# Kernel optimization log

Hardware: AMD Instinct MI355X
Metric: run time of the kernel (lower is better)

The kernel has to match this reference:

```python
import jax, jax.numpy as jnp
import numpy as np

B, D, H, W, C = 2, 128, 128, 128, 4
OD, OH, OW = 96, 96, 96
RANK = 3


def setup_inputs() -> dict:
    key = jax.random.key(0)
    k1, k2 = jax.random.split(key)
    inputs = jax.random.normal(k1, (B, D, H, W, C), dtype=jnp.float32)
    # continuous sample coords in [0, size-1] per spatial dim
    scale = jnp.array([D - 1, H - 1, W - 1], dtype=jnp.float32)
    sample_coords = jax.random.uniform(k2, (B, OD, OH, OW, RANK), dtype=jnp.float32) * scale
    return {"inputs": inputs, "sample_coords": sample_coords}


def _pyramid_combination(samples, w_0, w_1):
    # recursive weighted blend over 2^rank corner samples (matches TF module)
    if len(w_0) == 1:
        return samples[0] * w_1[0] + samples[1] * w_0[0]
    f_0 = _pyramid_combination(samples[::2], w_0[:-1], w_1[:-1])
    f_1 = _pyramid_combination(samples[1::2], w_0[:-1], w_1[:-1])
    return f_0 * w_1[-1] + f_1 * w_0[-1]


def reference(inputs, sample_coords):
    # inputs: [B, D, H, W, C]; sample_coords: [B, od, oh, ow, 3]
    in_spatial = inputs.shape[1:-1]
    rank = len(in_spatial)
    batch = inputs.shape[0]

    coords = [sample_coords[..., d] for d in range(rank)]          # each [B, od, oh, ow]
    base = [jnp.floor(c) for c in coords]
    # ZERO boundary -> replicate clamp of integer coords
    floor_i = [jnp.clip(b.astype(jnp.int32), 0, in_spatial[d] - 1) for d, b in enumerate(base)]
    ceil_i = [jnp.clip((b + 1.0).astype(jnp.int32), 0, in_spatial[d] - 1) for d, b in enumerate(base)]

    # ZERO-boundary weights use the CLAMPED corner coords (faithful to source)
    w_0 = [(c - f.astype(jnp.float32))[..., None] for c, f in zip(coords, floor_i)]
    w_1 = [(ce.astype(jnp.float32) - c)[..., None] for c, ce in zip(coords, ceil_i)]

    bids = jnp.arange(batch)[:, None, None, None]                  # broadcast batch ids
    sc = (floor_i, ceil_i)

    samples = []
    for i in range(2 ** rank):
        bits = [(i >> (rank - 1 - d)) & 1 for d in range(rank)]    # dim-0 is most significant bit
        idx = [sc[bits[d]][d] for d in range(rank)]
        samples.append(inputs[bids, idx[0], idx[1], idx[2]])       # [B, od, oh, ow, C]

    return _pyramid_combination(samples, w_0, w_1)
```

## Files before the change

### kernel.cpp

```cpp
#include <hip/hip_runtime.h>
#include <hip/hip_fp16.h>


constexpr int D = 128, H = 128, W = 128;
constexpr int OD = 96, OH = 96, OW = 96;
constexpr int VOX_PER_B = OD * OH * OW;
constexpr int NVOX = 2 * VOX_PER_B;

constexpr int NBINS = 1024;
constexpr int NB1 = 216;
constexpr int SPB = 8192;
constexpr int GT = 512;
constexpr int TILE_ELEMS = 9 * 5 * 128;

constexpr size_t OFF_MATRIX  = 0;
constexpr size_t OFF_NCNT    = (size_t)NB1 * NBINS * 4;
constexpr size_t OFF_BASE    = OFF_NCNT + NBINS * 4;
constexpr size_t OFF_RECORDS = OFF_BASE + NBINS * 4;
constexpr size_t WS_REQUIRED = OFF_RECORDS + (size_t)NVOX * 16;

__device__ __forceinline__ int bin_of(float cz, float cy, int b) {
    int z0 = min(max((int)floorf(cz), 0), D - 1);
    int y0 = min(max((int)floorf(cy), 0), H - 1);
    return (((b << 4) | (z0 >> 3)) << 5) | (y0 >> 2);
}

__device__ __forceinline__ float4 f4_fma(float w, float4 a, float4 acc) {
    acc.x = fmaf(w, a.x, acc.x);
    acc.y = fmaf(w, a.y, acc.y);
    acc.z = fmaf(w, a.z, acc.z);
    acc.w = fmaf(w, a.w, acc.w);
    return acc;
}
__device__ __forceinline__ float4 f4_scale(float w, float4 a) {
    return make_float4(w * a.x, w * a.y, w * a.z, w * a.w);
}

__device__ __forceinline__ float4 xblend(uint2 p0, uint2 p1, float w0, float w1) {
    const __half2 a0 = *(const __half2*)&p0.x;
    const __half2 a1 = *(const __half2*)&p0.y;
    const __half2 b0 = *(const __half2*)&p1.x;
    const __half2 b1 = *(const __half2*)&p1.y;
    const float2 A0 = __half22float2(a0), A1 = __half22float2(a1);
    const float2 B0 = __half22float2(b0), B1 = __half22float2(b1);
    float4 o;
    o.x = fmaf(w1, B0.x, w0 * A0.x);
    o.y = fmaf(w1, B0.y, w0 * A0.y);
    o.z = fmaf(w1, B1.x, w0 * A1.x);
    o.w = fmaf(w1, B1.y, w0 * A1.y);
    return o;
}

__global__ __launch_bounds__(1024) void hist_kernel(const float* __restrict__ coords,
                                                    unsigned* __restrict__ matrix) {
    __shared__ unsigned cnt[NBINS];
    const int t = threadIdx.x;
    cnt[t] = 0;
    __syncthreads();
    const int s0 = blockIdx.x * SPB;
#pragma unroll
    for (int j = 0; j < 8; j++) {
        const int s = s0 + j * 1024 + t;
        const float cz = coords[s * 3 + 0];
        const float cy = coords[s * 3 + 1];
        const int b = (s >= VOX_PER_B) ? 1 : 0;
        atomicAdd(&cnt[bin_of(cz, cy, b)], 1u);
    }
    __syncthreads();
    matrix[blockIdx.x * NBINS + t] = cnt[t];
}

__global__ __launch_bounds__(256) void scanA_kernel(unsigned* __restrict__ matrix,
                                                    unsigned* __restrict__ ncnt) {
    const int k = blockIdx.x;
    const int t = threadIdx.x;
    const unsigned v = (t < NB1) ? matrix[t * NBINS + k] : 0u;
    __shared__ unsigned s[256];
    s[t] = v;
    __syncthreads();
    for (int off = 1; off < 256; off <<= 1) {
        unsigned u = (t >= off) ? s[t - off] : 0u;
        __syncthreads();
        s[t] += u;
        __syncthreads();
    }
    if (t < NB1) matrix[t * NBINS + k] = s[t] - v;
    if (t == 255) ncnt[k] = s[255];
}

__global__ __launch_bounds__(1024) void scanB_kernel(const unsigned* __restrict__ ncnt,
                                                     unsigned* __restrict__ base) {
    const int t = threadIdx.x;
    const unsigned v = ncnt[t];
    __shared__ unsigned s[NBINS];
    s[t] = v;
    __syncthreads();
    for (int off = 1; off < NBINS; off <<= 1) {
        unsigned u = (t >= off) ? s[t - off] : 0u;
        __syncthreads();
        s[t] += u;
        __syncthreads();
    }
    base[t] = s[t] - v;
}

__global__ __launch_bounds__(1024) void scatter_kernel(const float* __restrict__ coords,
                                                       const unsigned* __restrict__ matrix,
                                                       const unsigned* __restrict__ base,
                                                       float4* __restrict__ records) {
    __shared__ float4 rec[SPB];
    __shared__ unsigned short binid[SPB];
    __shared__ unsigned cnt[NBINS];
    __shared__ unsigned pref[NBINS];
    __shared__ unsigned gb[NBINS];
    const int t = threadIdx.x;
    const int blk = blockIdx.x;
    cnt[t] = 0;
    gb[t] = base[t] + matrix[blk * NBINS + t];
    __syncthreads();

    const int s0 = blk * SPB;
    float czr[8], cyr[8], cxr[8];
    unsigned rankr[8];
#pragma unroll
    for (int j = 0; j < 8; j++) {
        const int s = s0 + j * 1024 + t;
        czr[j] = coords[s * 3 + 0];
        cyr[j] = coords[s * 3 + 1];
        cxr[j] = coords[s * 3 + 2];
        const int b = (s >= VOX_PER_B) ? 1 : 0;
        rankr[j] = atomicAdd(&cnt[bin_of(czr[j], cyr[j], b)], 1u);
    }
    __syncthreads();

    pref[t] = cnt[t];
    __syncthreads();
    for (int off = 1; off < NBINS; off <<= 1) {
        unsigned u = (t >= off) ? pref[t - off] : 0u;
        __syncthreads();
        pref[t] += u;
        __syncthreads();
    }
    {
        unsigned ex = pref[t] - cnt[t];
        __syncthreads();
        pref[t] = ex;
    }
    __syncthreads();

#pragma unroll
    for (int j = 0; j < 8; j++) {
        const int s = s0 + j * 1024 + t;
        const int b = (s >= VOX_PER_B) ? 1 : 0;
        const int k = bin_of(czr[j], cyr[j], b);
        const unsigned slot = pref[k] + rankr[j];
        rec[slot] = make_float4(czr[j], cyr[j], cxr[j], __uint_as_float((unsigned)s));
        binid[slot] = (unsigned short)k;
    }
    __syncthreads();

#pragma unroll
    for (int j = 0; j < 8; j++) {
        const int i = j * 1024 + t;
        const int k = binid[i];
        records[gb[k] + (unsigned)(i - (int)pref[k])] = rec[i];
    }
}

__global__ __launch_bounds__(GT) void gather_kernel(
    const float* __restrict__ inp,
    const float4* __restrict__ records,
    const unsigned* __restrict__ base,
    const unsigned* __restrict__ ncnt,
    float4* __restrict__ out)
{
    __shared__ uint2 tile[TILE_ELEMS];
    const int k = ((blockIdx.x & 7) << 7) | (blockIdx.x >> 3);
    const int b  = k >> 9;
    const int zb = (k >> 5) & 15;
    const int yb = k & 31;
    const int t = threadIdx.x;

    const float4* bp = (const float4*)inp + ((size_t)b << 21);
    const int zlim = min(9, D - zb * 8);
    const int ylim = min(5, H - yb * 4);
    for (int i = t; i < TILE_ELEMS; i += GT) {
        const int z = i / 640;
        const int r = i - z * 640;
        const int y = r >> 7;
        const int x = r & 127;
        if (z < zlim && y < ylim) {
            const float4 v = bp[((zb * 8 + z) << 14) | ((yb * 4 + y) << 7) | x];
            const __half2 lo = __floats2half2_rn(v.x, v.y);
            const __half2 hi = __floats2half2_rn(v.z, v.w);
            tile[i] = make_uint2(*(const unsigned*)&lo, *(const unsigned*)&hi);
        }
    }
    __syncthreads();

    const unsigned st = base[k];
    const unsigned n = ncnt[k];
    const int zoff = zb * 8, yoff = yb * 4;
    for (unsigned i = st + t; i < st + n; i += GT) {
        const float4 r = records[i];
        const float cz = r.x, cy = r.y, cx = r.z;
        const unsigned idx = __float_as_uint(r.w);

        const int z0 = (int)floorf(cz);
        const int y0 = (int)floorf(cy);
        const int x0 = (int)floorf(cx);

        const float wz0 = (float)(z0 + 1) - cz, wz1 = cz - (float)z0;
        const float wy0 = (float)(y0 + 1) - cy, wy1 = cy - (float)y0;
        const float wx0 = (float)(x0 + 1) - cx, wx1 = cx - (float)x0;

        const int a00 = (z0 - zoff) * 640 + (y0 - yoff) * 128 + x0;
        const int a01 = a00 + 128;
        const int a10 = a00 + 640;
        const int a11 = a00 + 768;

        const float4 c00 = xblend(tile[a00], tile[a00 + 1], wx0, wx1);
        const float4 c01 = xblend(tile[a01], tile[a01 + 1], wx0, wx1);
        const float4 c10 = xblend(tile[a10], tile[a10 + 1], wx0, wx1);
        const float4 c11 = xblend(tile[a11], tile[a11 + 1], wx0, wx1);

        const float4 c0 = f4_fma(wy1, c01, f4_scale(wy0, c00));
        const float4 c1 = f4_fma(wy1, c11, f4_scale(wy0, c10));
        out[idx] = f4_fma(wz1, c1, f4_scale(wz0, c0));
    }
}

__global__ __launch_bounds__(256) void direct_kernel(const float* __restrict__ inp,
                                                     const float* __restrict__ coords,
                                                     float4* __restrict__ out) {
    const int idx = blockIdx.x * 256 + threadIdx.x;
    if (idx >= NVOX) return;
    const float cz = coords[idx * 3 + 0];
    const float cy = coords[idx * 3 + 1];
    const float cx = coords[idx * 3 + 2];
    const int b = (idx >= VOX_PER_B) ? 1 : 0;

    const int fz = (int)floorf(cz);
    const int fy = (int)floorf(cy);
    const int fx = (int)floorf(cx);
    const int z1 = min(max(fz + 1, 0), D - 1);
    const int y1 = min(max(fy + 1, 0), H - 1);
    const int x1 = min(max(fx + 1, 0), W - 1);
    const int z0 = min(max(fz, 0), D - 1);
    const int y0 = min(max(fy, 0), H - 1);
    const int x0 = min(max(fx, 0), W - 1);
    const float wz0 = (float)z1 - cz, wz1 = cz - (float)z0;
    const float wy0 = (float)y1 - cy, wy1 = cy - (float)y0;
    const float wx0 = (float)x1 - cx, wx1 = cx - (float)x0;
    const float4* bp = (const float4*)inp + ((size_t)b << 21);
    const int z0o = z0 << 14, z1o = z1 << 14;
    const int y0o = y0 << 7,  y1o = y1 << 7;
    const float4 s000 = bp[z0o | y0o | x0];
    const float4 s001 = bp[z0o | y0o | x1];
    const float4 s010 = bp[z0o | y1o | x0];
    const float4 s011 = bp[z0o | y1o | x1];
    const float4 s100 = bp[z1o | y0o | x0];
    const float4 s101 = bp[z1o | y0o | x1];
    const float4 s110 = bp[z1o | y1o | x0];
    const float4 s111 = bp[z1o | y1o | x1];
    float4 c00 = f4_fma(wx1, s001, f4_scale(wx0, s000));
    float4 c01 = f4_fma(wx1, s011, f4_scale(wx0, s010));
    float4 c10 = f4_fma(wx1, s101, f4_scale(wx0, s100));
    float4 c11 = f4_fma(wx1, s111, f4_scale(wx0, s110));
    float4 c0 = f4_fma(wy1, c01, f4_scale(wy0, c00));
    float4 c1 = f4_fma(wy1, c11, f4_scale(wy0, c10));
    out[idx] = f4_fma(wz1, c1, f4_scale(wz0, c0));
}

extern "C" void kernel_launch(void* const* d_in, const int* in_sizes, int n_in,
                              void* d_out, int out_size, void* d_ws, size_t ws_size,
                              hipStream_t stream) {
    const float* inp    = (const float*)d_in[0];
    const float* coords = (const float*)d_in[1];
    float4* out = (float4*)d_out;

    if (ws_size < WS_REQUIRED) {
        direct_kernel<<<(NVOX + 255) / 256, 256, 0, stream>>>(inp, coords, out);
        return;
    }

    char* ws = (char*)d_ws;
    unsigned* matrix  = (unsigned*)(ws + OFF_MATRIX);
    unsigned* ncnt    = (unsigned*)(ws + OFF_NCNT);
    unsigned* base    = (unsigned*)(ws + OFF_BASE);
    float4*   records = (float4*)(ws + OFF_RECORDS);

    hist_kernel   <<<NB1, 1024, 0, stream>>>(coords, matrix);
    scanA_kernel  <<<NBINS, 256, 0, stream>>>(matrix, ncnt);
    scanB_kernel  <<<1, 1024, 0, stream>>>(ncnt, base);
    scatter_kernel<<<NB1, 1024, 0, stream>>>(coords, matrix, base, records);
    gather_kernel <<<NBINS, GT, 0, stream>>>(inp, records, base, ncnt, out);
}
```

Before: 173.8 us.

## Replace histogram and scan passes with atomic-reserved fixed-capacity bins and packed records

Removes the separate histogram and two scan kernels. Each scatter block now reserves space in fixed-capacity per-bin slots using global atomics, and writes compact 12-byte records holding the sample index, local floor offsets and 16-bit quantized fractions. If a bin overflows, the sample is interpolated directly inside the scatter kernel. This cuts two kernel launches and one full pass over the coordinates, and shrinks record traffic. In exchange it quantizes the interpolation weights to 16 bits and adds a memset plus possible slow paths when a bin overflows.

```diff
diff --git a/kernel.cpp b/kernel.cpp
--- a/kernel.cpp
+++ b/kernel.cpp
@@ -8,22 +8,17 @@
 constexpr int NVOX = 2 * VOX_PER_B;
 
 constexpr int NBINS = 1024;
+constexpr int CAP = 2048;
 constexpr int NB1 = 216;
 constexpr int SPB = 8192;
 constexpr int GT = 512;
 constexpr int TILE_ELEMS = 9 * 5 * 128;
 
-constexpr size_t OFF_MATRIX  = 0;
-constexpr size_t OFF_NCNT    = (size_t)NB1 * NBINS * 4;
-constexpr size_t OFF_BASE    = OFF_NCNT + NBINS * 4;
-constexpr size_t OFF_RECORDS = OFF_BASE + NBINS * 4;
-constexpr size_t WS_REQUIRED = OFF_RECORDS + (size_t)NVOX * 16;
-
-__device__ __forceinline__ int bin_of(float cz, float cy, int b) {
-    int z0 = min(max((int)floorf(cz), 0), D - 1);
-    int y0 = min(max((int)floorf(cy), 0), H - 1);
-    return (((b << 4) | (z0 >> 3)) << 5) | (y0 >> 2);
-}
+struct Rec { unsigned w0, w1, w2; };
+
+constexpr size_t OFF_GCNT    = 0;
+constexpr size_t OFF_RECORDS = 4096;
+constexpr size_t WS_REQUIRED = OFF_RECORDS + (size_t)NBINS * CAP * 12;
 
 __device__ __forceinline__ float4 f4_fma(float w, float4 a, float4 acc) {
     acc.x = fmaf(w, a.x, acc.x);
@@ -51,195 +46,8 @@
     return o;
 }
 
-__global__ __launch_bounds__(1024) void hist_kernel(const float* __restrict__ coords,
-                                                    unsigned* __restrict__ matrix) {
-    __shared__ unsigned cnt[NBINS];
-    const int t = threadIdx.x;
-    cnt[t] = 0;
-    __syncthreads();
-    const int s0 = blockIdx.x * SPB;
-#pragma unroll
-    for (int j = 0; j < 8; j++) {
-        const int s = s0 + j * 1024 + t;
-        const float cz = coords[s * 3 + 0];
-        const float cy = coords[s * 3 + 1];
-        const int b = (s >= VOX_PER_B) ? 1 : 0;
-        atomicAdd(&cnt[bin_of(cz, cy, b)], 1u);
-    }
-    __syncthreads();
-    matrix[blockIdx.x * NBINS + t] = cnt[t];
-}
-
-__global__ __launch_bounds__(256) void scanA_kernel(unsigned* __restrict__ matrix,
-                                                    unsigned* __restrict__ ncnt) {
-    const int k = blockIdx.x;
-    const int t = threadIdx.x;
-    const unsigned v = (t < NB1) ? matrix[t * NBINS + k] : 0u;
-    __shared__ unsigned s[256];
-    s[t] = v;
-    __syncthreads();
-    for (int off = 1; off < 256; off <<= 1) {
-        unsigned u = (t >= off) ? s[t - off] : 0u;
-        __syncthreads();
-        s[t] += u;
-        __syncthreads();
-    }
-    if (t < NB1) matrix[t * NBINS + k] = s[t] - v;
-    if (t == 255) ncnt[k] = s[255];
-}
-
-__global__ __launch_bounds__(1024) void scanB_kernel(const unsigned* __restrict__ ncnt,
-                                                     unsigned* __restrict__ base) {
-    const int t = threadIdx.x;
-    const unsigned v = ncnt[t];
-    __shared__ unsigned s[NBINS];
-    s[t] = v;
-    __syncthreads();
-    for (int off = 1; off < NBINS; off <<= 1) {
-        unsigned u = (t >= off) ? s[t - off] : 0u;
-        __syncthreads();
-        s[t] += u;
-        __syncthreads();
-    }
-    base[t] = s[t] - v;
-}
-
-__global__ __launch_bounds__(1024) void scatter_kernel(const float* __restrict__ coords,
-                                                       const unsigned* __restrict__ matrix,
-                                                       const unsigned* __restrict__ base,
-                                                       float4* __restrict__ records) {
-    __shared__ float4 rec[SPB];
-    __shared__ unsigned short binid[SPB];
-    __shared__ unsigned cnt[NBINS];
-    __shared__ unsigned pref[NBINS];
-    __shared__ unsigned gb[NBINS];
-    const int t = threadIdx.x;
-    const int blk = blockIdx.x;
-    cnt[t] = 0;
-    gb[t] = base[t] + matrix[blk * NBINS + t];
-    __syncthreads();
-
-    const int s0 = blk * SPB;
-    float czr[8], cyr[8], cxr[8];
-    unsigned rankr[8];
-#pragma unroll
-    for (int j = 0; j < 8; j++) {
-        const int s = s0 + j * 1024 + t;
-        czr[j] = coords[s * 3 + 0];
-        cyr[j] = coords[s * 3 + 1];
-        cxr[j] = coords[s * 3 + 2];
-        const int b = (s >= VOX_PER_B) ? 1 : 0;
-        rankr[j] = atomicAdd(&cnt[bin_of(czr[j], cyr[j], b)], 1u);
-    }
-    __syncthreads();
-
-    pref[t] = cnt[t];
-    __syncthreads();
-    for (int off = 1; off < NBINS; off <<= 1) {
-        unsigned u = (t >= off) ? pref[t - off] : 0u;
-        __syncthreads();
-        pref[t] += u;
-        __syncthreads();
-    }
-    {
-        unsigned ex = pref[t] - cnt[t];
-        __syncthreads();
-        pref[t] = ex;
-    }
-    __syncthreads();
-
-#pragma unroll
-    for (int j = 0; j < 8; j++) {
-        const int s = s0 + j * 1024 + t;
-        const int b = (s >= VOX_PER_B) ? 1 : 0;
-        const int k = bin_of(czr[j], cyr[j], b);
-        const unsigned slot = pref[k] + rankr[j];
-        rec[slot] = make_float4(czr[j], cyr[j], cxr[j], __uint_as_float((unsigned)s));
-        binid[slot] = (unsigned short)k;
-    }
-    __syncthreads();
-
-#pragma unroll
-    for (int j = 0; j < 8; j++) {
-        const int i = j * 1024 + t;
-        const int k = binid[i];
-        records[gb[k] + (unsigned)(i - (int)pref[k])] = rec[i];
-    }
-}
-
-__global__ __launch_bounds__(GT) void gather_kernel(
-    const float* __restrict__ inp,
-    const float4* __restrict__ records,
-    const unsigned* __restrict__ base,
-    const unsigned* __restrict__ ncnt,
-    float4* __restrict__ out)
-{
-    __shared__ uint2 tile[TILE_ELEMS];
-    const int k = ((blockIdx.x & 7) << 7) | (blockIdx.x >> 3);
-    const int b  = k >> 9;
-    const int zb = (k >> 5) & 15;
-    const int yb = k & 31;
-    const int t = threadIdx.x;
-
-    const float4* bp = (const float4*)inp + ((size_t)b << 21);
-    const int zlim = min(9, D - zb * 8);
-    const int ylim = min(5, H - yb * 4);
-    for (int i = t; i < TILE_ELEMS; i += GT) {
-        const int z = i / 640;
-        const int r = i - z * 640;
-        const int y = r >> 7;
-        const int x = r & 127;
-        if (z < zlim && y < ylim) {
-            const float4 v = bp[((zb * 8 + z) << 14) | ((yb * 4 + y) << 7) | x];
-            const __half2 lo = __floats2half2_rn(v.x, v.y);
-            const __half2 hi = __floats2half2_rn(v.z, v.w);
-            tile[i] = make_uint2(*(const unsigned*)&lo, *(const unsigned*)&hi);
-        }
-    }
-    __syncthreads();
-
-    const unsigned st = base[k];
-    const unsigned n = ncnt[k];
-    const int zoff = zb * 8, yoff = yb * 4;
-    for (unsigned i = st + t; i < st + n; i += GT) {
-        const float4 r = records[i];
-        const float cz = r.x, cy = r.y, cx = r.z;
-        const unsigned idx = __float_as_uint(r.w);
-
-        const int z0 = (int)floorf(cz);
-        const int y0 = (int)floorf(cy);
-        const int x0 = (int)floorf(cx);
-
-        const float wz0 = (float)(z0 + 1) - cz, wz1 = cz - (float)z0;
-        const float wy0 = (float)(y0 + 1) - cy, wy1 = cy - (float)y0;
-        const float wx0 = (float)(x0 + 1) - cx, wx1 = cx - (float)x0;
-
-        const int a00 = (z0 - zoff) * 640 + (y0 - yoff) * 128 + x0;
-        const int a01 = a00 + 128;
-        const int a10 = a00 + 640;
-        const int a11 = a00 + 768;
-
-        const float4 c00 = xblend(tile[a00], tile[a00 + 1], wx0, wx1);
-        const float4 c01 = xblend(tile[a01], tile[a01 + 1], wx0, wx1);
-        const float4 c10 = xblend(tile[a10], tile[a10 + 1], wx0, wx1);
-        const float4 c11 = xblend(tile[a11], tile[a11 + 1], wx0, wx1);
-
-        const float4 c0 = f4_fma(wy1, c01, f4_scale(wy0, c00));
-        const float4 c1 = f4_fma(wy1, c11, f4_scale(wy0, c10));
-        out[idx] = f4_fma(wz1, c1, f4_scale(wz0, c0));
-    }
-}
-
-__global__ __launch_bounds__(256) void direct_kernel(const float* __restrict__ inp,
-                                                     const float* __restrict__ coords,
-                                                     float4* __restrict__ out) {
-    const int idx = blockIdx.x * 256 + threadIdx.x;
-    if (idx >= NVOX) return;
-    const float cz = coords[idx * 3 + 0];
-    const float cy = coords[idx * 3 + 1];
-    const float cx = coords[idx * 3 + 2];
-    const int b = (idx >= VOX_PER_B) ? 1 : 0;
-
+__device__ __forceinline__ float4 trilinear(const float* __restrict__ inp,
+                                            float cz, float cy, float cx, int b) {
     const int fz = (int)floorf(cz);
     const int fy = (int)floorf(cy);
     const int fx = (int)floorf(cx);
@@ -269,7 +77,168 @@
     float4 c11 = f4_fma(wx1, s111, f4_scale(wx0, s110));
     float4 c0 = f4_fma(wy1, c01, f4_scale(wy0, c00));
     float4 c1 = f4_fma(wy1, c11, f4_scale(wy0, c10));
-    out[idx] = f4_fma(wz1, c1, f4_scale(wz0, c0));
+    return f4_fma(wz1, c1, f4_scale(wz0, c0));
+}
+
+__global__ __launch_bounds__(1024) void fused_scatter_kernel(
+    const float* __restrict__ coords,
+    const float* __restrict__ inp,
+    unsigned* __restrict__ gcnt,
+    Rec* __restrict__ records,
+    float4* __restrict__ out)
+{
+    __shared__ Rec rec[SPB];
+    __shared__ unsigned short binid[SPB];
+    __shared__ unsigned cnt[NBINS];
+    __shared__ unsigned pref[NBINS];
+    __shared__ unsigned gb[NBINS];
+    __shared__ unsigned s[1024];
+    const int t = threadIdx.x;
+    cnt[t] = 0;
+    __syncthreads();
+
+    const int s0 = blockIdx.x * SPB;
+    unsigned w0r[8], w1r[8], w2r[8], rankr[8];
+    int kr[8];
+#pragma unroll
+    for (int j = 0; j < 8; j++) {
+        const int smp = s0 + j * 1024 + t;
+        const float cz = coords[smp * 3 + 0];
+        const float cy = coords[smp * 3 + 1];
+        const float cx = coords[smp * 3 + 2];
+        const int b = (smp >= VOX_PER_B) ? 1 : 0;
+        const int z0 = (int)floorf(cz);
+        const int y0 = (int)floorf(cy);
+        const int x0 = (int)floorf(cx);
+        const unsigned fzq = min((unsigned)((cz - (float)z0) * 65536.0f), 65535u);
+        const unsigned fyq = min((unsigned)((cy - (float)y0) * 65536.0f), 65535u);
+        const unsigned fxq = min((unsigned)((cx - (float)x0) * 65536.0f), 65535u);
+        const int k = (b << 9) | ((z0 >> 3) << 5) | (y0 >> 2);
+        kr[j] = k;
+        w0r[j] = (unsigned)smp | ((unsigned)(z0 & 7) << 21) | ((unsigned)(y0 & 3) << 24);
+        w1r[j] = fzq | (fyq << 16);
+        w2r[j] = fxq | ((unsigned)x0 << 16);
+        rankr[j] = atomicAdd(&cnt[k], 1u);
+    }
+    __syncthreads();
+
+    pref[t] = cnt[t];
+    __syncthreads();
+    for (int off = 1; off < NBINS; off <<= 1) {
+        unsigned u = (t >= off) ? pref[t - off] : 0u;
+        __syncthreads();
+        pref[t] += u;
+        __syncthreads();
+    }
+    {
+        unsigned ex = pref[t] - cnt[t];
+        __syncthreads();
+        pref[t] = ex;
+    }
+    gb[t] = atomicAdd(&gcnt[t], cnt[t]);
+    __syncthreads();
+
+#pragma unroll
+    for (int j = 0; j < 8; j++) {
+        const unsigned slot = pref[kr[j]] + rankr[j];
+        rec[slot].w0 = w0r[j];
+        rec[slot].w1 = w1r[j];
+        rec[slot].w2 = w2r[j];
+        binid[slot] = (unsigned short)kr[j];
+    }
+    __syncthreads();
+
+#pragma unroll
+    for (int j = 0; j < 8; j++) {
+        const int i = j * 1024 + t;
+        const int k = binid[i];
+        const unsigned pos = gb[k] + (unsigned)(i - (int)pref[k]);
+        const Rec r = rec[i];
+        if (pos < (unsigned)CAP) {
+            records[(size_t)k * CAP + pos] = r;
+        } else {
+            const unsigned idx = r.w0 & 0x1FFFFFu;
+            const int b  = k >> 9;
+            const int z0 = ((k >> 5) & 15) * 8 + (int)((r.w0 >> 21) & 7u);
+            const int y0 = (k & 31) * 4 + (int)((r.w0 >> 24) & 3u);
+            const int x0 = (int)(r.w2 >> 16) & 127;
+            const float cz = (float)z0 + (float)(r.w1 & 0xFFFFu) * (1.0f / 65536.0f);
+            const float cy = (float)y0 + (float)(r.w1 >> 16) * (1.0f / 65536.0f);
+            const float cx = (float)x0 + (float)(r.w2 & 0xFFFFu) * (1.0f / 65536.0f);
+            out[idx] = trilinear(inp, cz, cy, cx, b);
+        }
+    }
+}
+
+__global__ __launch_bounds__(GT) void gather_kernel(
+    const float* __restrict__ inp,
+    const Rec* __restrict__ records,
+    const unsigned* __restrict__ gcnt,
+    float4* __restrict__ out)
+{
+    __shared__ uint2 tile[TILE_ELEMS];
+    const int k = ((blockIdx.x & 7) << 7) | (blockIdx.x >> 3);
+    const int b  = k >> 9;
+    const int zb = (k >> 5) & 15;
+    const int yb = k & 31;
+    const int t = threadIdx.x;
+
+    const float4* bp = (const float4*)inp + ((size_t)b << 21);
+    const int zlim = min(9, D - zb * 8);
+    const int ylim = min(5, H - yb * 4);
+    for (int i = t; i < TILE_ELEMS; i += GT) {
+        const int z = i / 640;
+        const int r = i - z * 640;
+        const int y = r >> 7;
+        const int x = r & 127;
+        if (z < zlim && y < ylim) {
+            const float4 v = bp[((zb * 8 + z) << 14) | ((yb * 4 + y) << 7) | x];
+            const __half2 lo = __floats2half2_rn(v.x, v.y);
+            const __half2 hi = __floats2half2_rn(v.z, v.w);
+            tile[i] = make_uint2(*(const unsigned*)&lo, *(const unsigned*)&hi);
+        }
+    }
+    __syncthreads();
+
+    const unsigned n = min(gcnt[k], (unsigned)CAP);
+    const Rec* rbase = records + (size_t)k * CAP;
+    for (unsigned i = t; i < n; i += GT) {
+        const Rec r = rbase[i];
+        const unsigned idx = r.w0 & 0x1FFFFFu;
+        const int z0l = (int)((r.w0 >> 21) & 7u);
+        const int y0l = (int)((r.w0 >> 24) & 3u);
+        const int x0  = (int)(r.w2 >> 16) & 127;
+        const float wz1 = (float)(r.w1 & 0xFFFFu) * (1.0f / 65536.0f);
+        const float wy1 = (float)(r.w1 >> 16) * (1.0f / 65536.0f);
+        const float wx1 = (float)(r.w2 & 0xFFFFu) * (1.0f / 65536.0f);
+        const float wz0 = 1.0f - wz1, wy0 = 1.0f - wy1, wx0 = 1.0f - wx1;
+
+        const int a00 = z0l * 640 + y0l * 128 + x0;
+        const int a01 = a00 + 128;
+        const int a10 = a00 + 640;
+        const int a11 = a00 + 768;
+
+        const float4 c00 = xblend(tile[a00], tile[a00 + 1], wx0, wx1);
+        const float4 c01 = xblend(tile[a01], tile[a01 + 1], wx0, wx1);
+        const float4 c10 = xblend(tile[a10], tile[a10 + 1], wx0, wx1);
+        const float4 c11 = xblend(tile[a11], tile[a11 + 1], wx0, wx1);
+
+        const float4 c0 = f4_fma(wy1, c01, f4_scale(wy0, c00));
+        const float4 c1 = f4_fma(wy1, c11, f4_scale(wy0, c10));
+        out[idx] = f4_fma(wz1, c1, f4_scale(wz0, c0));
+    }
+}
+
+__global__ __launch_bounds__(256) void direct_kernel(const float* __restrict__ inp,
+                                                     const float* __restrict__ coords,
+                                                     float4* __restrict__ out) {
+    const int idx = blockIdx.x * 256 + threadIdx.x;
+    if (idx >= NVOX) return;
+    const float cz = coords[idx * 3 + 0];
+    const float cy = coords[idx * 3 + 1];
+    const float cx = coords[idx * 3 + 2];
+    const int b = (idx >= VOX_PER_B) ? 1 : 0;
+    out[idx] = trilinear(inp, cz, cy, cx, b);
 }
 
 extern "C" void kernel_launch(void* const* d_in, const int* in_sizes, int n_in,
@@ -285,14 +254,10 @@
     }
 
     char* ws = (char*)d_ws;
-    unsigned* matrix  = (unsigned*)(ws + OFF_MATRIX);
-    unsigned* ncnt    = (unsigned*)(ws + OFF_NCNT);
-    unsigned* base    = (unsigned*)(ws + OFF_BASE);
-    float4*   records = (float4*)(ws + OFF_RECORDS);
-
-    hist_kernel   <<<NB1, 1024, 0, stream>>>(coords, matrix);
-    scanA_kernel  <<<NBINS, 256, 0, stream>>>(matrix, ncnt);
-    scanB_kernel  <<<1, 1024, 0, stream>>>(ncnt, base);
-    scatter_kernel<<<NB1, 1024, 0, stream>>>(coords, matrix, base, records);
-    gather_kernel <<<NBINS, GT, 0, stream>>>(inp, records, base, ncnt, out);
-}
+    unsigned* gcnt    = (unsigned*)(ws + OFF_GCNT);
+    Rec*      records = (Rec*)(ws + OFF_RECORDS);
+
+    hipMemsetAsync(gcnt, 0, NBINS * sizeof(unsigned), stream);
+    fused_scatter_kernel<<<NB1, 1024, 0, stream>>>(coords, inp, gcnt, records, out);
+    gather_kernel<<<NBINS, GT, 0, stream>>>(inp, records, gcnt, out);
+}
```

Measured after the change: 169.1 us. -2.7%, faster.
